# Kernel optimization log

Measured on AMD Instinct MI355X. Metric: run time of the kernel, lower is better.

## Reference

```python
import jax, jax.numpy as jnp
import numpy as np

# ---- hyperparameters (from init_kwargs) ----
SIGMA, RHO = 1.0, 10.0
ALPHA, BETA = 1.0, 1.0
K = 3  # ksize; patches are non-overlapping KxK, structure tensor computed on each patch
GRAY_W = np.array([0.2989, 0.587, 0.114], dtype=np.float32)  # torchvision Grayscale weights


def _gauss1d(sigma):
    d = np.arange(-1.0, 2.0, dtype=np.float32)  # radius-1 kernel (fits 3x3 patches)
    g = np.exp(-d * d / (2.0 * sigma * sigma))
    return (g / g.sum()).astype(np.float32)


def _dgauss1d(sigma):
    d = np.arange(-1.0, 2.0, dtype=np.float32)
    g = _gauss1d(sigma)
    return (-d / (sigma * sigma) * g).astype(np.float32)


def _conv3(x, k2d):
    # 'same' zero-padded 3x3 correlation over the last two dims, fully broadcast
    H, W = x.shape[-2], x.shape[-1]
    xp = jnp.pad(x, [(0, 0)] * (x.ndim - 2) + [(1, 1), (1, 1)])
    out = jnp.zeros_like(x)
    for i in range(3):
        for j in range(3):
            out = out + k2d[i, j] * xp[..., i:i + H, j:j + W]
    return out


# precomputed separable kernels (numpy constants)
_G_S, _DG_S, _G_R = _gauss1d(SIGMA), _dgauss1d(SIGMA), _gauss1d(RHO)
_KX = np.outer(_G_S, _DG_S)   # d/dx (last axis), gaussian-smoothed
_KY = np.outer(_DG_S, _G_S)   # d/dy
_KS = np.outer(_G_R, _G_R)    # rho smoothing


def _structure_tensor(gray):
    # gray: (..., K, K) -> (..., 3, K, K) components (Jxx, Jyy, Jxy)
    Ix = _conv3(gray, _KX)
    Iy = _conv3(gray, _KY)
    Jxx = _conv3(Ix * Ix, _KS)
    Jyy = _conv3(Iy * Iy, _KS)
    Jxy = _conv3(Ix * Iy, _KS)
    return jnp.stack([Jxx, Jyy, Jxy], axis=-3)


def _compute_patches(img):
    # img: (B, 3, H, W) -> (B, P, 3*K*K); non-overlapping KxK patches,
    # grayscale -> structure tensor -> per-patch L2 normalize (vectorized, no vmap-of-tiny-ops)
    B, C, H, W = img.shape
    Hb, Wb = H // K, W // K
    p = img.reshape(B, C, Hb, K, Wb, K).transpose(0, 2, 4, 1, 3, 5)  # (B,Hb,Wb,3,K,K)
    p = p.reshape(B, Hb * Wb, C, K, K)
    gray = jnp.einsum('bpchw,c->bphw', p, jnp.asarray(GRAY_W, p.dtype))
    st = _structure_tensor(gray)                                      # (B,P,3,K,K)
    n = jnp.sqrt(jnp.sum(st * st, axis=(-3, -2, -1), keepdims=True)) + 1e-12
    st = st / n
    return st.reshape(B, Hb * Wb, 3 * K * K)


def _resize(img, factor):
    B, C, H, W = img.shape
    return jax.image.resize(img, (B, C, int(H * factor), int(W * factor)),
                            method='bicubic', antialias=False)


def _pairdist_sq(a, b):
    # squared L2 pairwise distance (monotone in L2; only used for argmin)
    aa = jnp.sum(a * a, axis=-1)[:, :, None]
    bb = jnp.sum(b * b, axis=-1)[:, None, :]
    ab = jnp.einsum('bnw,bmw->bnm', a, b)
    return aa + bb - 2.0 * ab


def _loss(x, gt):
    p1 = _compute_patches(x)
    p2 = _compute_patches(gt)
    p2_2 = _compute_patches(_resize(gt, 0.5))
    p2_4 = _compute_patches(_resize(gt, 0.25))
    p2c = jnp.concatenate([p2, p2_2, p2_4], axis=1)      # (B, P2cat, 27)
    score = ALPHA * _pairdist_sq(p1, p2c) + BETA * _pairdist_sq(p2, p2c)
    ind = jnp.argmin(score, axis=2)                      # (B, P1) nearest-neighbor indices
    sel = jnp.take_along_axis(p2c, ind[:, :, None], axis=1)
    return jnp.mean(jnp.abs(p1 - sel))                   # L1 criterion


def setup_inputs() -> dict:
    key = jax.random.key(0)
    k1, k2 = jax.random.split(key)
    x = jax.random.uniform(k1, (4, 3, 192, 192), dtype=jnp.float32)
    gt = jax.random.uniform(k2, (4, 3, 192, 192), dtype=jnp.float32)
    return {'x': x, 'gt': gt}


def reference(x, gt):
    return _loss(x, gt)
```

## Files before the change

### kernel.cpp

```cpp
#include <hip/hip_runtime.h>
#include <hip/hip_bf16.h>
#include <math.h>

namespace {
constexpr int BATCH = 4;
constexpr int IMG   = 192;
constexpr int PL    = IMG * IMG;
constexpr int NP1   = 4096;
constexpr int MALL  = 5376;
constexpr int RS    = 28;
constexpr int NCHUNK = 21;
constexpr int TPC    = 16;
constexpr int RPT    = 2;
constexpr int ROUNDS = TPC / RPT;
constexpr int NROWS  = BATCH * NP1;

#define GA 0.27406862f
#define GB 0.45186276f
#define RC 0.33277732f
#define RD 0.33444537f

typedef __bf16 bf16x8 __attribute__((ext_vector_type(8)));
typedef float  f32x4  __attribute__((ext_vector_type(4)));

__device__ __forceinline__ void conv3(const float in[9], const float k[9], float out[9]) {
#pragma unroll
  for (int y = 0; y < 3; ++y)
#pragma unroll
    for (int x = 0; x < 3; ++x) {
      float s = 0.f;
#pragma unroll
      for (int i = 0; i < 3; ++i) {
        int yy = y + i - 1;
        if (yy < 0 || yy > 2) continue;
#pragma unroll
        for (int j = 0; j < 3; ++j) {
          int xx = x + j - 1;
          if (xx < 0 || xx > 2) continue;
          s = fmaf(k[i * 3 + j], in[yy * 3 + xx], s);
        }
      }
      out[y * 3 + x] = s;
    }
}

__device__ __forceinline__ void st_from_gray(const float gray[9], float stv[27], float& cs) {
  const float KX[9] = {GA * GA, 0.f, -GA * GA, GB * GA, 0.f, -GB * GA, GA * GA, 0.f, -GA * GA};
  const float KY[9] = {GA * GA, GA * GB, GA * GA, 0.f, 0.f, 0.f, -GA * GA, -GA * GB, -GA * GA};
  const float KS[9] = {RC * RC, RC * RD, RC * RC, RD * RC, RD * RD, RD * RC, RC * RC, RC * RD, RC * RC};
  float Ix[9], Iy[9];
  conv3(gray, KX, Ix);
  conv3(gray, KY, Iy);
  float Pxx[9], Pyy[9], Pxy[9];
#pragma unroll
  for (int t = 0; t < 9; ++t) {
    Pxx[t] = Ix[t] * Ix[t];
    Pyy[t] = Iy[t] * Iy[t];
    Pxy[t] = Ix[t] * Iy[t];
  }
  conv3(Pxx, KS, stv + 0);
  conv3(Pyy, KS, stv + 9);
  conv3(Pxy, KS, stv + 18);
  float s2 = 0.f;
#pragma unroll
  for (int d = 0; d < 27; ++d) s2 = fmaf(stv[d], stv[d], s2);
  float inv = 1.0f / (sqrtf(s2) + 1e-12f);
  float c = 0.f;
#pragma unroll
  for (int d = 0; d < 27; ++d) {
    stv[d] *= inv;
    c = fmaf(stv[d], stv[d], c);
  }
  cs = c;
}

__device__ __forceinline__ void mkw(int k0, int IS, float w[4], int k[4]) {
  const float W4[4] = {-0.0625f, 0.5625f, 0.5625f, -0.0625f};
  float ssum = 0.f;
#pragma unroll
  for (int u = 0; u < 4; ++u) {
    int kk = k0 + u;
    bool v = (kk >= 0) && (kk < IS);
    w[u] = v ? W4[u] : 0.f;
    k[u] = v ? kk : 0;
    ssum += w[u];
  }
  float inv = 1.f / ssum;
#pragma unroll
  for (int u = 0; u < 4; ++u) w[u] *= inv;
}

__device__ __forceinline__ void pack_row_frag(const float* __restrict__ v, float tail,
                                              unsigned* __restrict__ base, int rl) {
  unsigned uh[16], ul[16];
#pragma unroll
  for (int p = 0; p < 16; ++p) {
    float a  = (2 * p < 27) ? v[2 * p] : 0.f;
    float bb = (2 * p + 1 < 27) ? v[2 * p + 1] : (2 * p + 1 == 27 ? tail : 0.f);
    __hip_bfloat16 ah = __float2bfloat16(a);
    __hip_bfloat16 bh = __float2bfloat16(bb);
    float af = __bfloat162float(ah), bf2 = __bfloat162float(bh);
    __hip_bfloat16 al = __float2bfloat16(a - af);
    __hip_bfloat16 bl = __float2bfloat16(bb - bf2);
    uh[p] = ((unsigned)__builtin_bit_cast(unsigned short, bh) << 16) |
            (unsigned)__builtin_bit_cast(unsigned short, ah);
    ul[p] = ((unsigned)__builtin_bit_cast(unsigned short, bl) << 16) |
            (unsigned)__builtin_bit_cast(unsigned short, al);
  }
#pragma unroll
  for (int lg = 0; lg < 4; ++lg) {
    *reinterpret_cast<uint4*>(base + (size_t)(lg * 16 + rl) * 4) =
        make_uint4(uh[4 * lg], uh[4 * lg + 1], uh[4 * lg + 2], uh[4 * lg + 3]);
    *reinterpret_cast<uint4*>(base + 256 + (size_t)(lg * 16 + rl) * 4) =
        make_uint4(ul[4 * lg], ul[4 * lg + 1], ul[4 * lg + 2], ul[4 * lg + 3]);
  }
}

__device__ __forceinline__ void store_row28(float* __restrict__ dst, const float v[27], float tail) {
  float4* d4 = reinterpret_cast<float4*>(dst);
#pragma unroll
  for (int i = 0; i < 6; ++i)
    d4[i] = make_float4(v[4 * i], v[4 * i + 1], v[4 * i + 2], v[4 * i + 3]);
  d4[6] = make_float4(v[24], v[25], v[26], tail);
}

__global__ void __launch_bounds__(256) gray_kernel(
    const float* __restrict__ x, const float* __restrict__ gt,
    float* __restrict__ gx, float* __restrict__ ggt, unsigned* __restrict__ ctr) {
  int o = blockIdx.x * 256 + threadIdx.x;
  if (o == 0) ctr[0] = 0;
  const float* src;
  float* dst;
  int oo;
  if (o < BATCH * PL) { src = x; dst = gx; oo = o; }
  else                { src = gt; dst = ggt; oo = o - BATCH * PL; }
  int b = oo / PL, p = oo - b * PL;
  const float* im = src + (size_t)b * 3 * PL;
  dst[oo] = fmaf(0.114f, im[2 * PL + p], fmaf(0.587f, im[PL + p], 0.2989f * im[p]));
}

__global__ void __launch_bounds__(256) resize_gray_kernel(
    const float* __restrict__ ggt, float* __restrict__ g96, float* __restrict__ g48) {
  int o = blockIdx.x * 256 + threadIdx.x;
  int i, j, step, koff;
  const float* src;
  float* dst;
  int oo;
  if (o < BATCH * 9216) {
    int b = o / 9216, rem = o - b * 9216;
    i = rem / 96; j = rem - i * 96;
    step = 2; koff = -1;
    src = ggt + (size_t)b * PL;
    dst = g96; oo = o;
  } else {
    int q = o - BATCH * 9216;
    int b = q / 2304, rem = q - b * 2304;
    i = rem / 48; j = rem - i * 48;
    step = 4; koff = 0;
    src = ggt + (size_t)b * PL;
    dst = g48; oo = q;
  }
  float wr[4], wc[4];
  int kr[4], kc[4];
  mkw(step * i + koff, IMG, wr, kr);
  mkw(step * j + koff, IMG, wc, kc);
  float acc = 0.f;
#pragma unroll
  for (int u = 0; u < 4; ++u) {
    float rs = 0.f;
#pragma unroll
    for (int v = 0; v < 4; ++v) rs = fmaf(wc[v], src[kr[u] * IMG + kc[v]], rs);
    acc = fmaf(wr[u], rs, acc);
  }
  dst[oo] = acc;
}

__global__ void __launch_bounds__(256) patch_all_kernel(
    const float* __restrict__ gx, const float* __restrict__ ggt,
    const float* __restrict__ g96, const float* __restrict__ g48,
    float* __restrict__ p1, float* __restrict__ p2c,
    unsigned* __restrict__ Qp, unsigned* __restrict__ Cp) {
  int g = blockIdx.x * 256 + threadIdx.x;
  if (g < 2 * NROWS) {
    const int pid = g >> 1;
    const bool isgt = g & 1;
    const int b = pid >> 12, p = pid & (NP1 - 1);
    const int hb = p >> 6, wb = p & 63;
    const float* src = (isgt ? ggt : gx) + (size_t)b * PL + (hb * 3) * IMG + wb * 3;
    float gr[9];
#pragma unroll
    for (int y = 0; y < 3; ++y)
#pragma unroll
      for (int xx = 0; xx < 3; ++xx) gr[y * 3 + xx] = src[y * IMG + xx];
    float s[27];
    float cs;
    st_from_gray(gr, s, cs);

    float o27[27];
#pragma unroll
    for (int d = 0; d < 27; ++d) o27[d] = __shfl_xor(s[d], 1, 64);

    if (!isgt) {
      store_row28(p1 + (size_t)pid * RS, s, cs);
    } else {
      size_t crow = (size_t)b * MALL + p;
      store_row28(p2c + crow * RS, s, cs);
      pack_row_frag(s, -cs, Cp + (crow >> 4) * 512, (int)(crow & 15));
      float q[27];
#pragma unroll
      for (int d = 0; d < 27; ++d) q[d] = s[d] + o27[d];
      pack_row_frag(q, 1.0f, Qp + (size_t)(pid >> 4) * 512, pid & 15);
    }
  } else {
    int q = g - 2 * NROWS;
    const float* src;
    int S, row, hb, wb;
    if (q < BATCH * 1024) {
      int b = q >> 10, p = q & 1023;
      hb = p >> 5; wb = p & 31;
      src = g96 + (size_t)b * 9216;
      S = 96;
      row = b * MALL + NP1 + p;
    } else {
      int q2 = q - BATCH * 1024;
      int b = q2 >> 8, p = q2 & 255;
      hb = p >> 4; wb = p & 15;
      src = g48 + (size_t)b * 2304;
      S = 48;
      row = b * MALL + NP1 + 1024 + p;
    }
    float gr[9];
#pragma unroll
    for (int y = 0; y < 3; ++y)
#pragma unroll
      for (int xx = 0; xx < 3; ++xx) gr[y * 3 + xx] = src[(3 * hb + y) * S + 3 * wb + xx];
    float s[27];
    float cs;
    st_from_gray(gr, s, cs);
    store_row28(p2c + (size_t)row * RS, s, cs);
    pack_row_frag(s, -cs, Cp + ((size_t)row >> 4) * 512, row & 15);
  }
}

__global__ void __launch_bounds__(256) argmin_mfma_kernel(
    const unsigned* __restrict__ Qp, const unsigned* __restrict__ Cp,
    unsigned* __restrict__ pkey, int* __restrict__ pidx) {
  const int lane = threadIdx.x & 63;
  const int w = threadIdx.x >> 6;
  const int td = threadIdx.x;
  const int chunk = blockIdx.y;
  const int b = blockIdx.z;
  const int nbase = blockIdx.x * 256 + w * 64;
  const int lm = lane & 15, lg = lane >> 4;

  __shared__ unsigned cbuf[2][RPT * 512];

  bf16x8 qh[4], ql[4];
#pragma unroll
  for (int t = 0; t < 4; ++t) {
    const unsigned* tb = Qp + (size_t)((b * NP1 + nbase) >> 4) * 512 + (size_t)t * 512 + lane * 4;
    qh[t] = *reinterpret_cast<const bf16x8*>(tb);
    ql[t] = *reinterpret_cast<const bf16x8*>(tb + 256);
  }

  unsigned keys[4][4];
#pragma unroll
  for (int t = 0; t < 4; ++t)
#pragma unroll
    for (int r = 0; r < 4; ++r) keys[t][r] = 0u;

  const int tile0 = chunk * TPC;
  const unsigned* ct = Cp + (size_t)(b * (MALL >> 4) + tile0) * 512;

  {
    uint2 a0 = *reinterpret_cast<const uint2*>(ct + 2 * td);
    uint2 a1 = *reinterpret_cast<const uint2*>(ct + 512 + 2 * td);
    *reinterpret_cast<uint2*>(&cbuf[0][2 * td]) = a0;
    *reinterpret_cast<uint2*>(&cbuf[0][512 + 2 * td]) = a1;
  }
  __syncthreads();

  for (int r = 0; r < ROUNDS; ++r) {
    uint2 n0, n1;
    if (r + 1 < ROUNDS) {
      const unsigned* nt = ct + (size_t)(r + 1) * (RPT * 512);
      n0 = *reinterpret_cast<const uint2*>(nt + 2 * td);
      n1 = *reinterpret_cast<const uint2*>(nt + 512 + 2 * td);
    }
    const unsigned* cbr = &cbuf[r & 1][0];
#pragma unroll
    for (int it = 0; it < RPT; ++it) {
      const int i = r * RPT + it;
      bf16x8 ch = *reinterpret_cast<const bf16x8*>(cbr + it * 512 + lane * 4);
      bf16x8 cl = *reinterpret_cast<const bf16x8*>(cbr + it * 512 + 256 + lane * 4);
      const unsigned tag = (unsigned)(TPC - 1 - i);
#pragma unroll
      for (int t = 0; t < 4; ++t) {
        f32x4 a = {4.f, 4.f, 4.f, 4.f};
        a = __builtin_amdgcn_mfma_f32_16x16x32_bf16(qh[t], ch, a, 0, 0, 0);
        a = __builtin_amdgcn_mfma_f32_16x16x32_bf16(ql[t], ch, a, 0, 0, 0);
        a = __builtin_amdgcn_mfma_f32_16x16x32_bf16(qh[t], cl, a, 0, 0, 0);
#pragma unroll
        for (int rr = 0; rr < 4; ++rr) {
          unsigned kb = (__builtin_bit_cast(unsigned, (float)a[rr]) & 0xFFFFFFE0u) | tag;
          keys[t][rr] = keys[t][rr] > kb ? keys[t][rr] : kb;
        }
      }
    }
    if (r + 1 < ROUNDS) {
      __syncthreads();
      *reinterpret_cast<uint2*>(&cbuf[(r + 1) & 1][2 * td]) = n0;
      *reinterpret_cast<uint2*>(&cbuf[(r + 1) & 1][512 + 2 * td]) = n1;
      __syncthreads();
    }
  }

#pragma unroll
  for (int t = 0; t < 4; ++t)
#pragma unroll
    for (int r = 0; r < 4; ++r) {
      unsigned k = keys[t][r];
      int m = (tile0 + (int)((unsigned)(TPC - 1) - (k & 31u))) * 16 + lm;
#pragma unroll
      for (int mk = 1; mk < 16; mk <<= 1) {
        unsigned ok = (unsigned)__shfl_xor((int)k, mk, 64);
        int om = __shfl_xor(m, mk, 64);
        bool take = (ok > k) || (ok == k && om < m);
        k = take ? ok : k;
        m = take ? om : m;
      }
      if (lm == 0) {
        int row = nbase + t * 16 + lg * 4 + r;
        size_t o = (size_t)chunk * NROWS + b * NP1 + row;
        pkey[o] = k & 0xFFFFFFE0u;
        pidx[o] = m;
      }
    }
}

__global__ void __launch_bounds__(256) finalize_kernel(
    const float* __restrict__ p1, const float* __restrict__ p2c,
    const unsigned* __restrict__ pkey, const int* __restrict__ pidx,
    float* __restrict__ bsum, unsigned* __restrict__ ctr, float* __restrict__ out) {
  int g = blockIdx.x * 256 + threadIdx.x;
  unsigned bk = 0u;
  int bi = 0;
  for (int ms = 0; ms < NCHUNK; ++ms) {
    unsigned k = pkey[(size_t)ms * NROWS + g];
    int ix = pidx[(size_t)ms * NROWS + g];
    bool gg = k > bk;
    bk = gg ? k : bk;
    bi = gg ? ix : bi;
  }
  int b = g >> 12;
  const float* a = p1 + (size_t)g * RS;
  const float* s2 = p2c + ((size_t)b * MALL + bi) * RS;
  float acc = 0.f;
#pragma unroll
  for (int d = 0; d < 27; ++d) acc += fabsf(a[d] - s2[d]);

  __shared__ float red[256];
  red[threadIdx.x] = acc;
  __syncthreads();
  for (int st = 128; st > 0; st >>= 1) {
    if (threadIdx.x < st) red[threadIdx.x] += red[threadIdx.x + st];
    __syncthreads();
  }
  if (threadIdx.x == 0) {
    __hip_atomic_store(&bsum[blockIdx.x], red[0], __ATOMIC_RELEASE, __HIP_MEMORY_SCOPE_AGENT);
    unsigned prev = __hip_atomic_fetch_add(ctr, 1u, __ATOMIC_ACQ_REL, __HIP_MEMORY_SCOPE_AGENT);
    if (prev == 63) {
      float s = 0.f;
      for (int i = 0; i < 64; ++i)
        s += __hip_atomic_load(&bsum[i], __ATOMIC_ACQUIRE, __HIP_MEMORY_SCOPE_AGENT);
      out[0] = s * (1.0f / 442368.0f);
    }
  }
}

}

extern "C" void kernel_launch(void* const* d_in, const int* in_sizes, int n_in,
                              void* d_out, int out_size, void* d_ws, size_t ws_size,
                              hipStream_t stream) {
  const float* x  = (const float*)d_in[0];
  const float* gt = (const float*)d_in[1];
  float* out = (float*)d_out;

  float* ws = (float*)d_ws;
  float* p1   = ws;
  float* p2c  = p1 + (size_t)BATCH * NP1 * RS;
  unsigned* Qp = (unsigned*)(p2c + (size_t)BATCH * MALL * RS);
  unsigned* Cp = Qp + (size_t)BATCH * NP1 * 32;
  float* gx   = (float*)(Cp + (size_t)BATCH * MALL * 32);
  float* ggt  = gx + (size_t)BATCH * PL;
  float* g96  = ggt + (size_t)BATCH * PL;
  float* g48  = g96 + (size_t)BATCH * 9216;
  unsigned* pkey = (unsigned*)(g48 + (size_t)BATCH * 2304);
  int*   pidx   = (int*)(pkey + (size_t)NCHUNK * NROWS);
  float* bsum   = (float*)(pidx + (size_t)NCHUNK * NROWS);
  unsigned* ctr = (unsigned*)(bsum + 64);

  gray_kernel<<<(2 * BATCH * PL) / 256, 256, 0, stream>>>(x, gt, gx, ggt, ctr);

  resize_gray_kernel<<<(BATCH * (9216 + 2304)) / 256, 256, 0, stream>>>(ggt, g96, g48);

  patch_all_kernel<<<(2 * NROWS + BATCH * 1280) / 256, 256, 0, stream>>>(
      gx, ggt, g96, g48, p1, p2c, Qp, Cp);

  {
    dim3 grid(16, NCHUNK, BATCH);
    argmin_mfma_kernel<<<grid, 256, 0, stream>>>(Qp, Cp, pkey, pidx);
  }

  finalize_kernel<<<64, 256, 0, stream>>>(p1, p2c, pkey, pidx, bsum, ctr, out);
}
```

Before: 63.57 us.

## Fuse grayscale and resize into patch kernel; fold finalize into argmin

Grayscale conversion and bicubic downsampling are now computed on the fly inside the patch kernel, so the separate gray and resize kernels and their intermediate buffers go away. The finalize reduction moves into the argmin kernel. The last chunk block for each row group, found through a per-group atomic counter, does the cross-chunk argmin merge and L1 sum. This cuts five launches to two and removes global round-trips of the gray images. In exchange, the resized patches redo bicubic and gray work from the 3-channel input, and the argmin tail adds fences and an atomic.

```diff
diff --git a/kernel.cpp b/kernel.cpp
--- a/kernel.cpp
+++ b/kernel.cpp
@@ -90,6 +90,27 @@
   for (int u = 0; u < 4; ++u) w[u] *= inv;
 }
 
+__device__ __forceinline__ float bicubic_gray(const float* __restrict__ im,
+                                              int i, int j, int step, int koff) {
+  float wr[4], wc[4];
+  int kr[4], kc[4];
+  mkw(step * i + koff, IMG, wr, kr);
+  mkw(step * j + koff, IMG, wc, kc);
+  float acc = 0.f;
+#pragma unroll
+  for (int u = 0; u < 4; ++u) {
+    float rs = 0.f;
+#pragma unroll
+    for (int v = 0; v < 4; ++v) {
+      int o = kr[u] * IMG + kc[v];
+      float gy = fmaf(0.114f, im[2 * PL + o], fmaf(0.587f, im[PL + o], 0.2989f * im[o]));
+      rs = fmaf(wc[v], gy, rs);
+    }
+    acc = fmaf(wr[u], rs, acc);
+  }
+  return acc;
+}
+
 __device__ __forceinline__ void pack_row_frag(const float* __restrict__ v, float tail,
                                               unsigned* __restrict__ base, int rl) {
   unsigned uh[16], ul[16];
@@ -124,74 +145,30 @@
   d4[6] = make_float4(v[24], v[25], v[26], tail);
 }
 
-__global__ void __launch_bounds__(256) gray_kernel(
+__global__ void __launch_bounds__(256) prep_all_kernel(
     const float* __restrict__ x, const float* __restrict__ gt,
-    float* __restrict__ gx, float* __restrict__ ggt, unsigned* __restrict__ ctr) {
-  int o = blockIdx.x * 256 + threadIdx.x;
-  if (o == 0) ctr[0] = 0;
-  const float* src;
-  float* dst;
-  int oo;
-  if (o < BATCH * PL) { src = x; dst = gx; oo = o; }
-  else                { src = gt; dst = ggt; oo = o - BATCH * PL; }
-  int b = oo / PL, p = oo - b * PL;
-  const float* im = src + (size_t)b * 3 * PL;
-  dst[oo] = fmaf(0.114f, im[2 * PL + p], fmaf(0.587f, im[PL + p], 0.2989f * im[p]));
-}
-
-__global__ void __launch_bounds__(256) resize_gray_kernel(
-    const float* __restrict__ ggt, float* __restrict__ g96, float* __restrict__ g48) {
-  int o = blockIdx.x * 256 + threadIdx.x;
-  int i, j, step, koff;
-  const float* src;
-  float* dst;
-  int oo;
-  if (o < BATCH * 9216) {
-    int b = o / 9216, rem = o - b * 9216;
-    i = rem / 96; j = rem - i * 96;
-    step = 2; koff = -1;
-    src = ggt + (size_t)b * PL;
-    dst = g96; oo = o;
-  } else {
-    int q = o - BATCH * 9216;
-    int b = q / 2304, rem = q - b * 2304;
-    i = rem / 48; j = rem - i * 48;
-    step = 4; koff = 0;
-    src = ggt + (size_t)b * PL;
-    dst = g48; oo = q;
-  }
-  float wr[4], wc[4];
-  int kr[4], kc[4];
-  mkw(step * i + koff, IMG, wr, kr);
-  mkw(step * j + koff, IMG, wc, kc);
-  float acc = 0.f;
-#pragma unroll
-  for (int u = 0; u < 4; ++u) {
-    float rs = 0.f;
-#pragma unroll
-    for (int v = 0; v < 4; ++v) rs = fmaf(wc[v], src[kr[u] * IMG + kc[v]], rs);
-    acc = fmaf(wr[u], rs, acc);
-  }
-  dst[oo] = acc;
-}
-
-__global__ void __launch_bounds__(256) patch_all_kernel(
-    const float* __restrict__ gx, const float* __restrict__ ggt,
-    const float* __restrict__ g96, const float* __restrict__ g48,
     float* __restrict__ p1, float* __restrict__ p2c,
-    unsigned* __restrict__ Qp, unsigned* __restrict__ Cp) {
+    unsigned* __restrict__ Qp, unsigned* __restrict__ Cp,
+    unsigned* __restrict__ gctr, unsigned* __restrict__ fctr) {
   int g = blockIdx.x * 256 + threadIdx.x;
+  if (g < 64) gctr[g] = 0;
+  if (g == 64) fctr[0] = 0;
+
   if (g < 2 * NROWS) {
     const int pid = g >> 1;
     const bool isgt = g & 1;
     const int b = pid >> 12, p = pid & (NP1 - 1);
     const int hb = p >> 6, wb = p & 63;
-    const float* src = (isgt ? ggt : gx) + (size_t)b * PL + (hb * 3) * IMG + wb * 3;
+    const float* src = (isgt ? gt : x) + (size_t)b * 3 * PL + (hb * 3) * IMG + wb * 3;
     float gr[9];
 #pragma unroll
     for (int y = 0; y < 3; ++y)
 #pragma unroll
-      for (int xx = 0; xx < 3; ++xx) gr[y * 3 + xx] = src[y * IMG + xx];
+      for (int xx = 0; xx < 3; ++xx) {
+        int o = y * IMG + xx;
+        gr[y * 3 + xx] = fmaf(0.114f, src[2 * PL + o],
+                              fmaf(0.587f, src[PL + o], 0.2989f * src[o]));
+      }
     float s[27];
     float cs;
     st_from_gray(gr, s, cs);
@@ -213,27 +190,28 @@
     }
   } else {
     int q = g - 2 * NROWS;
-    const float* src;
-    int S, row, hb, wb;
+    int row, hb, wb, step, koff;
+    const float* im;
     if (q < BATCH * 1024) {
       int b = q >> 10, p = q & 1023;
       hb = p >> 5; wb = p & 31;
-      src = g96 + (size_t)b * 9216;
-      S = 96;
+      im = gt + (size_t)b * 3 * PL;
+      step = 2; koff = -1;
       row = b * MALL + NP1 + p;
     } else {
       int q2 = q - BATCH * 1024;
       int b = q2 >> 8, p = q2 & 255;
       hb = p >> 4; wb = p & 15;
-      src = g48 + (size_t)b * 2304;
-      S = 48;
+      im = gt + (size_t)b * 3 * PL;
+      step = 4; koff = 0;
       row = b * MALL + NP1 + 1024 + p;
     }
     float gr[9];
 #pragma unroll
     for (int y = 0; y < 3; ++y)
 #pragma unroll
-      for (int xx = 0; xx < 3; ++xx) gr[y * 3 + xx] = src[(3 * hb + y) * S + 3 * wb + xx];
+      for (int xx = 0; xx < 3; ++xx)
+        gr[y * 3 + xx] = bicubic_gray(im, 3 * hb + y, 3 * wb + xx, step, koff);
     float s[27];
     float cs;
     st_from_gray(gr, s, cs);
@@ -244,7 +222,10 @@
 
 __global__ void __launch_bounds__(256) argmin_mfma_kernel(
     const unsigned* __restrict__ Qp, const unsigned* __restrict__ Cp,
-    unsigned* __restrict__ pkey, int* __restrict__ pidx) {
+    const float* __restrict__ p1, const float* __restrict__ p2c,
+    unsigned* __restrict__ pkey, int* __restrict__ pidx,
+    unsigned* __restrict__ gctr, float* __restrict__ bsum,
+    unsigned* __restrict__ fctr, float* __restrict__ out) {
   const int lane = threadIdx.x & 63;
   const int w = threadIdx.x >> 6;
   const int td = threadIdx.x;
@@ -254,6 +235,7 @@
   const int lm = lane & 15, lg = lane >> 4;
 
   __shared__ unsigned cbuf[2][RPT * 512];
+  __shared__ int sfin;
 
   bf16x8 qh[4], ql[4];
 #pragma unroll
@@ -336,13 +318,20 @@
         pidx[o] = m;
       }
     }
-}
-
-__global__ void __launch_bounds__(256) finalize_kernel(
-    const float* __restrict__ p1, const float* __restrict__ p2c,
-    const unsigned* __restrict__ pkey, const int* __restrict__ pidx,
-    float* __restrict__ bsum, unsigned* __restrict__ ctr, float* __restrict__ out) {
-  int g = blockIdx.x * 256 + threadIdx.x;
+
+  __syncthreads();
+  const int gid = b * 16 + blockIdx.x;
+  if (td == 0) {
+    __threadfence();
+    unsigned prev = __hip_atomic_fetch_add(&gctr[gid], 1u, __ATOMIC_ACQ_REL,
+                                           __HIP_MEMORY_SCOPE_AGENT);
+    sfin = (prev == NCHUNK - 1);
+  }
+  __syncthreads();
+  if (!sfin) return;
+  __threadfence();
+
+  const int g = gid * 256 + td;
   unsigned bk = 0u;
   int bi = 0;
   for (int ms = 0; ms < NCHUNK; ++ms) {
@@ -352,23 +341,23 @@
     bk = gg ? k : bk;
     bi = gg ? ix : bi;
   }
-  int b = g >> 12;
   const float* a = p1 + (size_t)g * RS;
   const float* s2 = p2c + ((size_t)b * MALL + bi) * RS;
   float acc = 0.f;
 #pragma unroll
   for (int d = 0; d < 27; ++d) acc += fabsf(a[d] - s2[d]);
 
-  __shared__ float red[256];
-  red[threadIdx.x] = acc;
+  float* red = reinterpret_cast<float*>(&cbuf[0][0]);
+  red[td] = acc;
   __syncthreads();
   for (int st = 128; st > 0; st >>= 1) {
-    if (threadIdx.x < st) red[threadIdx.x] += red[threadIdx.x + st];
+    if (td < st) red[td] += red[td + st];
     __syncthreads();
   }
-  if (threadIdx.x == 0) {
-    __hip_atomic_store(&bsum[blockIdx.x], red[0], __ATOMIC_RELEASE, __HIP_MEMORY_SCOPE_AGENT);
-    unsigned prev = __hip_atomic_fetch_add(ctr, 1u, __ATOMIC_ACQ_REL, __HIP_MEMORY_SCOPE_AGENT);
+  if (td == 0) {
+    __hip_atomic_store(&bsum[gid], red[0], __ATOMIC_RELEASE, __HIP_MEMORY_SCOPE_AGENT);
+    unsigned prev = __hip_atomic_fetch_add(fctr, 1u, __ATOMIC_ACQ_REL,
+                                           __HIP_MEMORY_SCOPE_AGENT);
     if (prev == 63) {
       float s = 0.f;
       for (int i = 0; i < 64; ++i)
@@ -392,26 +381,18 @@
   float* p2c  = p1 + (size_t)BATCH * NP1 * RS;
   unsigned* Qp = (unsigned*)(p2c + (size_t)BATCH * MALL * RS);
   unsigned* Cp = Qp + (size_t)BATCH * NP1 * 32;
-  float* gx   = (float*)(Cp + (size_t)BATCH * MALL * 32);
-  float* ggt  = gx + (size_t)BATCH * PL;
-  float* g96  = ggt + (size_t)BATCH * PL;
-  float* g48  = g96 + (size_t)BATCH * 9216;
-  unsigned* pkey = (unsigned*)(g48 + (size_t)BATCH * 2304);
+  unsigned* pkey = Cp + (size_t)BATCH * MALL * 32;
   int*   pidx   = (int*)(pkey + (size_t)NCHUNK * NROWS);
   float* bsum   = (float*)(pidx + (size_t)NCHUNK * NROWS);
-  unsigned* ctr = (unsigned*)(bsum + 64);
-
-  gray_kernel<<<(2 * BATCH * PL) / 256, 256, 0, stream>>>(x, gt, gx, ggt, ctr);
-
-  resize_gray_kernel<<<(BATCH * (9216 + 2304)) / 256, 256, 0, stream>>>(ggt, g96, g48);
-
-  patch_all_kernel<<<(2 * NROWS + BATCH * 1280) / 256, 256, 0, stream>>>(
-      gx, ggt, g96, g48, p1, p2c, Qp, Cp);
+  unsigned* gctr = (unsigned*)(bsum + 64);
+  unsigned* fctr = gctr + 64;
+
+  prep_all_kernel<<<(2 * NROWS + BATCH * 1280) / 256, 256, 0, stream>>>(
+      x, gt, p1, p2c, Qp, Cp, gctr, fctr);
 
   {
     dim3 grid(16, NCHUNK, BATCH);
-    argmin_mfma_kernel<<<grid, 256, 0, stream>>>(Qp, Cp, pkey, pidx);
-  }
-
-  finalize_kernel<<<64, 256, 0, stream>>>(p1, p2c, pkey, pidx, bsum, ctr, out);
-}
+    argmin_mfma_kernel<<<grid, 256, 0, stream>>>(
+        Qp, Cp, p1, p2c, pkey, pidx, gctr, bsum, fctr, out);
+  }
+}
```

After: 149.8 us. 136% more time.
